# Optimization experiments

Hardware: AMD Instinct MI355X
Metric: run time of the kernel (lower is better)

Reference implementation:

```python
import jax, jax.numpy as jnp
import numpy as np

NDIV = (10, 10)
OUT_CHANNEL = 100


def setup_inputs() -> dict:
    key = jax.random.key(0)
    k1, k2 = jax.random.split(key)
    x1 = jax.random.normal(k1, (8, 64, 128, 128), dtype=jnp.float32)
    x2 = jax.random.normal(k2, (8, 64, 60, 60), dtype=jnp.float32)
    return {"x1": x1, "x2": x2}


def reference(x1, x2):
    B, C, H, W = x1.shape
    h, w = x2.shape[-2], x2.shape[-1]
    nd0, nd1 = NDIV
    hh, ww = h // nd0, w // nd1  # patch size (6, 6)
    P = nd0 * nd1                # 100 patches per sample

    # channel-wise L2 normalization (dim=1)
    x1n = x1 / jnp.linalg.norm(x1, axis=1, keepdims=True)
    x2n = x2 / jnp.linalg.norm(x2, axis=1, keepdims=True)

    # extract nd0*nd1 patches per sample as conv filters: [B*P, C, hh, ww]
    patches = x2n.reshape(B, C, nd0, hh, nd1, ww)
    patches = patches.transpose(0, 2, 4, 1, 3, 5).reshape(B * P, C, hh, ww)

    # grouped cross-correlation (torch F.conv2d = correlation, no kernel flip)
    lhs = x1n.reshape(1, B * C, H, W)
    mm = jax.lax.conv_general_dilated(
        lhs, patches,
        window_strides=(1, 1),
        padding=((hh // 2, hh // 2), (ww // 2, ww // 2)),
        feature_group_count=B,
        dimension_numbers=("NCHW", "OIHW", "NCHW"),
    ) / (hh * ww)  # [1, B*P, H+1, W+1] for even hh,ww

    # bilinear resize to (H, W)  (torch align_corners=False == half-pixel)
    mm = jax.image.resize(mm, (1, B * P, H, W), method="bilinear")

    # [B, P, H, W] -> topk over patch dim, then mean
    mm = mm.reshape(B, P, H, W)
    topv = jax.lax.top_k(jnp.moveaxis(mm, 1, -1), OUT_CHANNEL)[0]  # [B,H,W,k]
    out = jnp.mean(topv, axis=-1)[:, None]  # [B,1,H,W]
    return out
```

## Files before the change

kernel.cpp:

```cpp
#include <hip/hip_runtime.h>
#include <cstddef>

#define BB   8
#define CC   64
#define H1   128
#define W1   128
#define HW1  (H1*W1)
#define HS   60
#define WS   60
#define HO   129
#define WO   129
#define NPIX (HS*WS)

#define UPL  (BB*HW1)

typedef _Float16 f16;

__global__ __launch_bounds__(256) void k_inv2(const float* __restrict__ x2,
                                              float* __restrict__ inv2) {
    int idx = blockIdx.x * 256 + threadIdx.x;
    if (idx >= BB * NPIX) return;
    int b  = idx / NPIX;
    int hw = idx - b * NPIX;
    const float* p = x2 + (size_t)b * CC * NPIX + hw;
    float s = 0.f;
#pragma unroll
    for (int cc = 0; cc < CC; cc += 8) {
        float v0 = p[(cc+0)*NPIX], v1 = p[(cc+1)*NPIX];
        float v2 = p[(cc+2)*NPIX], v3 = p[(cc+3)*NPIX];
        float v4 = p[(cc+4)*NPIX], v5 = p[(cc+5)*NPIX];
        float v6 = p[(cc+6)*NPIX], v7 = p[(cc+7)*NPIX];
        s += v0*v0 + v1*v1 + v2*v2 + v3*v3 + v4*v4 + v5*v5 + v6*v6 + v7*v7;
    }
    inv2[idx] = 1.0f / sqrtf(s);
}

__global__ __launch_bounds__(256) void k_fold(const float* __restrict__ x2,
                                              const float* __restrict__ inv2,
                                              float* __restrict__ S) {
    __shared__ float bins[36];
    int tid = threadIdx.x;
    int bc  = blockIdx.x;
    int b   = bc >> 6;
    if (tid < 36) bins[tid] = 0.f;
    __syncthreads();
    const float* px = x2 + (size_t)bc * NPIX;
    const float* pn = inv2 + b * NPIX;
    for (int i = tid; i < NPIX; i += 256) {
        int hh = i / WS, ww = i - hh * WS;
        int bin = (hh % 6) * 6 + (ww % 6);
        atomicAdd(&bins[bin], px[i] * pn[i]);
    }
    __syncthreads();
    if (tid < 36) S[bc * 36 + tid] = bins[tid];
}

__global__ __launch_bounds__(256) void k_gemm(const float* __restrict__ x1,
                                              const float* __restrict__ S,
                                              f16* __restrict__ U) {
    int b = blockIdx.x >> 6;
    int p = (blockIdx.x & 63) * 256 + threadIdx.x;

    const float* xp = x1 + (size_t)b * CC * HW1 + p;
    const float* Sb = S + (size_t)b * (CC * 36);

    float acc[36];
#pragma unroll
    for (int t = 0; t < 36; ++t) acc[t] = 0.f;
    float s2 = 0.f;

    for (int cc = 0; cc < CC; cc += 8) {
        float v[8];
#pragma unroll
        for (int j = 0; j < 8; ++j) v[j] = xp[(size_t)(cc + j) * HW1];
#pragma unroll
        for (int j = 0; j < 8; ++j) {
            const float* sj = Sb + (cc + j) * 36;
            float vv = v[j];
            s2 += vv * vv;
#pragma unroll
            for (int t = 0; t < 36; ++t) acc[t] += vv * sj[t];
        }
    }

    float inv = (1.0f / 3600.0f) / sqrtf(s2);
    f16* up = U + (size_t)b * HW1 + p;
#pragma unroll
    for (int t = 0; t < 36; ++t) up[(size_t)t * UPL] = (f16)(acc[t] * inv);
}

__global__ __launch_bounds__(256) void k_out(const f16* __restrict__ U,
                                             float* __restrict__ out) {
    __shared__ float m[20 * 21];
    int blk  = blockIdx.x;
    int b    = blk >> 6;
    int tile = blk & 63;
    int oy0 = (tile >> 3) * 16, ox0 = (tile & 7) * 16;
    int ry0 = oy0 - 1, rx0 = ox0 - 1;
    int tid = threadIdx.x;

    const f16* Ub = U + (size_t)b * HW1;

    for (int i = tid; i < 400; i += 256) {
        int ly = i / 20, lx = i - ly * 20;
        int jy = min(max(ry0 + ly, 0), 128);
        int jx = min(max(rx0 + lx, 0), 128);
        float s = 0.f;
#pragma unroll
        for (int t = 0; t < 36; ++t) {
            int dy = t / 6, dx = t - dy * 6;
            int py = jy - 3 + dy, px = jx - 3 + dx;
            if ((unsigned)py < 128u && (unsigned)px < 128u)
                s += (float)Ub[(size_t)t * UPL + py * W1 + px];
        }
        m[ly * 21 + lx] = s;
    }
    __syncthreads();

    const float inv_scale = 129.0f / 128.0f;
    const float ksc       = 128.0f / 129.0f;

    int oy = oy0 + (tid >> 4);
    int ox = ox0 + (tid & 15);

    float sy = (oy + 0.5f) * inv_scale - 0.5f;
    float sx = (ox + 0.5f) * inv_scale - 0.5f;
    int fy = (int)floorf(sy);
    int fx = (int)floorf(sx);

    float wy[4], wx[4];
    float sumy = 0.f, sumx = 0.f;
#pragma unroll
    for (int k = 0; k < 4; ++k) {
        int jy = fy - 1 + k;
        float w = 0.f;
        if (jy >= 0 && jy < HO) w = fmaxf(0.f, 1.0f - fabsf(sy - (float)jy) * ksc);
        wy[k] = w; sumy += w;
        int jx = fx - 1 + k;
        float w2 = 0.f;
        if (jx >= 0 && jx < WO) w2 = fmaxf(0.f, 1.0f - fabsf(sx - (float)jx) * ksc);
        wx[k] = w2; sumx += w2;
    }

    float r = 0.f;
#pragma unroll
    for (int ky = 0; ky < 4; ++ky) {
        if (wy[ky] == 0.f) continue;
        int ly = fy - 1 + ky - ry0;
        float rowv = 0.f;
#pragma unroll
        for (int kx = 0; kx < 4; ++kx) {
            if (wx[kx] == 0.f) continue;
            int lx = fx - 1 + kx - rx0;
            rowv += wx[kx] * m[ly * 21 + lx];
        }
        r += wy[ky] * rowv;
    }

    out[(size_t)b * HW1 + oy * W1 + ox] = r / (sumy * sumx);
}

extern "C" void kernel_launch(void* const* d_in, const int* in_sizes, int n_in,
                              void* d_out, int out_size, void* d_ws, size_t ws_size,
                              hipStream_t stream) {
    const float* x1 = (const float*)d_in[0];
    const float* x2 = (const float*)d_in[1];
    float* out = (float*)d_out;

    float* ws   = (float*)d_ws;
    float* inv2 = ws;
    float* Sbuf = inv2 + BB * NPIX;
    f16*   U    = (f16*)(Sbuf + BB * CC * 36);

    k_inv2<<<(BB * NPIX + 255) / 256, 256, 0, stream>>>(x2, inv2);
    k_fold<<<BB * CC, 256, 0, stream>>>(x2, inv2, Sbuf);
    k_gemm<<<BB * 64, 256, 0, stream>>>(x1, Sbuf, U);
    k_out <<<BB * 64, 256, 0, stream>>>(U, out);
}
```

Baseline: 128.4 us.

## Fuse all stages into one cooperative kernel with grid-wide syncs

Replaces the four separate launches with a single cooperative kernel of 512 blocks that runs the inverse-norm, patch-fold, GEMM and resize/output stages, separated by grid.sync barriers. The fold stage is restructured so each block handles a 4-row chunk of x2, with per-chunk partial bins that a second phase reduces instead of using LDS atomics. This targets per-launch overhead and the serialization between small kernels. In exchange it adds grid-barrier cost and depends on all 512 blocks being co-resident.

Result: slower. 347.4 us (+170.6%).

```diff
diff --git a/kernel.cpp b/kernel.cpp
--- a/kernel.cpp
+++ b/kernel.cpp
@@ -1,5 +1,8 @@
 #include <hip/hip_runtime.h>
+#include <hip/hip_cooperative_groups.h>
 #include <cstddef>
+
+namespace cg = cooperative_groups;
 
 #define BB   8
 #define CC   64
@@ -11,153 +14,169 @@
 #define HO   129
 #define WO   129
 #define NPIX (HS*WS)
+#define NCHUNK 15
 
 #define UPL  (BB*HW1)
 
 typedef _Float16 f16;
 
-__global__ __launch_bounds__(256) void k_inv2(const float* __restrict__ x2,
-                                              float* __restrict__ inv2) {
-    int idx = blockIdx.x * 256 + threadIdx.x;
-    if (idx >= BB * NPIX) return;
-    int b  = idx / NPIX;
-    int hw = idx - b * NPIX;
-    const float* p = x2 + (size_t)b * CC * NPIX + hw;
-    float s = 0.f;
+__global__ __launch_bounds__(256) void k_all(const float* __restrict__ x1,
+                                             const float* __restrict__ x2,
+                                             float* __restrict__ Spart,
+                                             float* __restrict__ S,
+                                             f16* __restrict__ U,
+                                             float* __restrict__ out) {
+    cg::grid_group grid = cg::this_grid();
+    __shared__ float lds[420];
+    int blk = blockIdx.x;
+    int tid = threadIdx.x;
+
+    if (blk < BB * NCHUNK) {
+        int b = blk / NCHUNK, chunk = blk - b * NCHUNK;
+        int px0 = chunk * 240;
+
+        if (tid < 240) {
+            const float* p = x2 + (size_t)b * CC * NPIX + px0 + tid;
+            float s = 0.f;
 #pragma unroll
-    for (int cc = 0; cc < CC; cc += 8) {
-        float v0 = p[(cc+0)*NPIX], v1 = p[(cc+1)*NPIX];
-        float v2 = p[(cc+2)*NPIX], v3 = p[(cc+3)*NPIX];
-        float v4 = p[(cc+4)*NPIX], v5 = p[(cc+5)*NPIX];
-        float v6 = p[(cc+6)*NPIX], v7 = p[(cc+7)*NPIX];
-        s += v0*v0 + v1*v1 + v2*v2 + v3*v3 + v4*v4 + v5*v5 + v6*v6 + v7*v7;
-    }
-    inv2[idx] = 1.0f / sqrtf(s);
-}
+            for (int c = 0; c < CC; ++c) { float v = p[c * NPIX]; s += v * v; }
+            lds[tid] = 1.0f / sqrtf(s);
+        }
+        __syncthreads();
 
-__global__ __launch_bounds__(256) void k_fold(const float* __restrict__ x2,
-                                              const float* __restrict__ inv2,
-                                              float* __restrict__ S) {
-    __shared__ float bins[36];
-    int tid = threadIdx.x;
-    int bc  = blockIdx.x;
-    int b   = bc >> 6;
-    if (tid < 36) bins[tid] = 0.f;
-    __syncthreads();
-    const float* px = x2 + (size_t)bc * NPIX;
-    const float* pn = inv2 + b * NPIX;
-    for (int i = tid; i < NPIX; i += 256) {
-        int hh = i / WS, ww = i - hh * WS;
-        int bin = (hh % 6) * 6 + (ww % 6);
-        atomicAdd(&bins[bin], px[i] * pn[i]);
-    }
-    __syncthreads();
-    if (tid < 36) S[bc * 36 + tid] = bins[tid];
-}
+        int c = tid >> 2, q = tid & 3;
+        int row = chunk * 4 + q;
+        const float* px = x2 + ((size_t)b * CC + c) * NPIX + row * WS;
+        const float* iv = lds + q * 60;
+        float acc[6] = {0, 0, 0, 0, 0, 0};
+#pragma unroll
+        for (int i = 0; i < 60; ++i)
+            acc[i % 6] += px[i] * iv[i];
 
-__global__ __launch_bounds__(256) void k_gemm(const float* __restrict__ x1,
-                                              const float* __restrict__ S,
-                                              f16* __restrict__ U) {
-    int b = blockIdx.x >> 6;
-    int p = (blockIdx.x & 63) * 256 + threadIdx.x;
-
-    const float* xp = x1 + (size_t)b * CC * HW1 + p;
-    const float* Sb = S + (size_t)b * (CC * 36);
-
-    float acc[36];
+        float* sb = Spart + (((size_t)b * CC + c) * NCHUNK + chunk) * 36;
+        int r0 = row % 6;
 #pragma unroll
-    for (int t = 0; t < 36; ++t) acc[t] = 0.f;
-    float s2 = 0.f;
-
-    for (int cc = 0; cc < CC; cc += 8) {
-        float v[8];
+        for (int j = 0; j < 6; ++j) sb[r0 * 6 + j] = acc[j];
+        if (q < 2) {
+            int rm = (chunk * 4 + 4 + q) % 6;
 #pragma unroll
-        for (int j = 0; j < 8; ++j) v[j] = xp[(size_t)(cc + j) * HW1];
-#pragma unroll
-        for (int j = 0; j < 8; ++j) {
-            const float* sj = Sb + (cc + j) * 36;
-            float vv = v[j];
-            s2 += vv * vv;
-#pragma unroll
-            for (int t = 0; t < 36; ++t) acc[t] += vv * sj[t];
+            for (int j = 0; j < 6; ++j) sb[rm * 6 + j] = 0.f;
         }
     }
+    grid.sync();
 
-    float inv = (1.0f / 3600.0f) / sqrtf(s2);
-    f16* up = U + (size_t)b * HW1 + p;
-#pragma unroll
-    for (int t = 0; t < 36; ++t) up[(size_t)t * UPL] = (f16)(acc[t] * inv);
-}
-
-__global__ __launch_bounds__(256) void k_out(const f16* __restrict__ U,
-                                             float* __restrict__ out) {
-    __shared__ float m[20 * 21];
-    int blk  = blockIdx.x;
-    int b    = blk >> 6;
-    int tile = blk & 63;
-    int oy0 = (tile >> 3) * 16, ox0 = (tile & 7) * 16;
-    int ry0 = oy0 - 1, rx0 = ox0 - 1;
-    int tid = threadIdx.x;
-
-    const f16* Ub = U + (size_t)b * HW1;
-
-    for (int i = tid; i < 400; i += 256) {
-        int ly = i / 20, lx = i - ly * 20;
-        int jy = min(max(ry0 + ly, 0), 128);
-        int jx = min(max(rx0 + lx, 0), 128);
+    if (blk < 72) {
+        int e = blk * 256 + tid;
+        int bc = e / 36, bin = e - bc * 36;
+        const float* sp = Spart + (size_t)bc * NCHUNK * 36 + bin;
         float s = 0.f;
 #pragma unroll
-        for (int t = 0; t < 36; ++t) {
-            int dy = t / 6, dx = t - dy * 6;
-            int py = jy - 3 + dy, px = jx - 3 + dx;
-            if ((unsigned)py < 128u && (unsigned)px < 128u)
-                s += (float)Ub[(size_t)t * UPL + py * W1 + px];
+        for (int k = 0; k < NCHUNK; ++k) s += sp[k * 36];
+        S[e] = s;
+    }
+    grid.sync();
+
+    {
+        int b = blk >> 6;
+        int p = (blk & 63) * 256 + tid;
+
+        const float* xp = x1 + (size_t)b * CC * HW1 + p;
+        const float* Sb = S + (size_t)b * (CC * 36);
+
+        float acc[36];
+#pragma unroll
+        for (int t = 0; t < 36; ++t) acc[t] = 0.f;
+        float s2 = 0.f;
+
+        for (int cc = 0; cc < CC; cc += 8) {
+            float v[8];
+#pragma unroll
+            for (int j = 0; j < 8; ++j) v[j] = xp[(size_t)(cc + j) * HW1];
+#pragma unroll
+            for (int j = 0; j < 8; ++j) {
+                const float* sj = Sb + (cc + j) * 36;
+                float vv = v[j];
+                s2 += vv * vv;
+#pragma unroll
+                for (int t = 0; t < 36; ++t) acc[t] += vv * sj[t];
+            }
         }
-        m[ly * 21 + lx] = s;
+
+        float inv = (1.0f / 3600.0f) / sqrtf(s2);
+        f16* up = U + (size_t)b * HW1 + p;
+#pragma unroll
+        for (int t = 0; t < 36; ++t) up[(size_t)t * UPL] = (f16)(acc[t] * inv);
     }
-    __syncthreads();
+    grid.sync();
 
-    const float inv_scale = 129.0f / 128.0f;
-    const float ksc       = 128.0f / 129.0f;
+    {
+        float* m = lds;
+        int b    = blk >> 6;
+        int tile = blk & 63;
+        int oy0 = (tile >> 3) * 16, ox0 = (tile & 7) * 16;
+        int ry0 = oy0 - 1, rx0 = ox0 - 1;
 
-    int oy = oy0 + (tid >> 4);
-    int ox = ox0 + (tid & 15);
+        const f16* Ub = U + (size_t)b * HW1;
 
-    float sy = (oy + 0.5f) * inv_scale - 0.5f;
-    float sx = (ox + 0.5f) * inv_scale - 0.5f;
-    int fy = (int)floorf(sy);
-    int fx = (int)floorf(sx);
+        __syncthreads();
+        for (int i = tid; i < 400; i += 256) {
+            int ly = i / 20, lx = i - ly * 20;
+            int jy = min(max(ry0 + ly, 0), 128);
+            int jx = min(max(rx0 + lx, 0), 128);
+            float s = 0.f;
+#pragma unroll
+            for (int t = 0; t < 36; ++t) {
+                int dy = t / 6, dx = t - dy * 6;
+                int py = jy - 3 + dy, px = jx - 3 + dx;
+                if ((unsigned)py < 128u && (unsigned)px < 128u)
+                    s += (float)Ub[(size_t)t * UPL + py * W1 + px];
+            }
+            m[ly * 21 + lx] = s;
+        }
+        __syncthreads();
 
-    float wy[4], wx[4];
-    float sumy = 0.f, sumx = 0.f;
+        const float inv_scale = 129.0f / 128.0f;
+        const float ksc       = 128.0f / 129.0f;
+
+        int oy = oy0 + (tid >> 4);
+        int ox = ox0 + (tid & 15);
+
+        float sy = (oy + 0.5f) * inv_scale - 0.5f;
+        float sx = (ox + 0.5f) * inv_scale - 0.5f;
+        int fy = (int)floorf(sy);
+        int fx = (int)floorf(sx);
+
+        float wy[4], wx[4];
+        float sumy = 0.f, sumx = 0.f;
 #pragma unroll
-    for (int k = 0; k < 4; ++k) {
-        int jy = fy - 1 + k;
-        float w = 0.f;
-        if (jy >= 0 && jy < HO) w = fmaxf(0.f, 1.0f - fabsf(sy - (float)jy) * ksc);
-        wy[k] = w; sumy += w;
-        int jx = fx - 1 + k;
-        float w2 = 0.f;
-        if (jx >= 0 && jx < WO) w2 = fmaxf(0.f, 1.0f - fabsf(sx - (float)jx) * ksc);
-        wx[k] = w2; sumx += w2;
+        for (int k = 0; k < 4; ++k) {
+            int jy = fy - 1 + k;
+            float w = 0.f;
+            if (jy >= 0 && jy < HO) w = fmaxf(0.f, 1.0f - fabsf(sy - (float)jy) * ksc);
+            wy[k] = w; sumy += w;
+            int jx = fx - 1 + k;
+            float w2 = 0.f;
+            if (jx >= 0 && jx < WO) w2 = fmaxf(0.f, 1.0f - fabsf(sx - (float)jx) * ksc);
+            wx[k] = w2; sumx += w2;
+        }
+
+        float r = 0.f;
+#pragma unroll
+        for (int ky = 0; ky < 4; ++ky) {
+            if (wy[ky] == 0.f) continue;
+            int ly = fy - 1 + ky - ry0;
+            float rowv = 0.f;
+#pragma unroll
+            for (int kx = 0; kx < 4; ++kx) {
+                if (wx[kx] == 0.f) continue;
+                int lx = fx - 1 + kx - rx0;
+                rowv += wx[kx] * m[ly * 21 + lx];
+            }
+            r += wy[ky] * rowv;
+        }
+
+        out[(size_t)b * HW1 + oy * W1 + ox] = r / (sumy * sumx);
     }
-
-    float r = 0.f;
-#pragma unroll
-    for (int ky = 0; ky < 4; ++ky) {
-        if (wy[ky] == 0.f) continue;
-        int ly = fy - 1 + ky - ry0;
-        float rowv = 0.f;
-#pragma unroll
-        for (int kx = 0; kx < 4; ++kx) {
-            if (wx[kx] == 0.f) continue;
-            int lx = fx - 1 + kx - rx0;
-            rowv += wx[kx] * m[ly * 21 + lx];
-        }
-        r += wy[ky] * rowv;
-    }
-
-    out[(size_t)b * HW1 + oy * W1 + ox] = r / (sumy * sumx);
 }
 
 extern "C" void kernel_launch(void* const* d_in, const int* in_sizes, int n_in,
@@ -167,13 +186,13 @@
     const float* x2 = (const float*)d_in[1];
     float* out = (float*)d_out;
 
-    float* ws   = (float*)d_ws;
-    float* inv2 = ws;
-    float* Sbuf = inv2 + BB * NPIX;
-    f16*   U    = (f16*)(Sbuf + BB * CC * 36);
+    float* ws    = (float*)d_ws;
+    float* Spart = ws;
+    float* S     = Spart + (size_t)BB * CC * NCHUNK * 36;
+    f16*   U     = (f16*)(S + BB * CC * 36);
 
-    k_inv2<<<(BB * NPIX + 255) / 256, 256, 0, stream>>>(x2, inv2);
-    k_fold<<<BB * CC, 256, 0, stream>>>(x2, inv2, Sbuf);
-    k_gemm<<<BB * 64, 256, 0, stream>>>(x1, Sbuf, U);
-    k_out <<<BB * 64, 256, 0, stream>>>(U, out);
+    void* args[] = {(void*)&x1, (void*)&x2, (void*)&Spart, (void*)&S,
+                    (void*)&U, (void*)&out};
+    hipLaunchCooperativeKernel((void*)k_all, dim3(512), dim3(256),
+                               args, 0, stream);
 }
```
